# Kernel tuning notes

Hardware: AMD Instinct MI355X
Metric: run time of the kernel (lower is better)

The kernel has to match this reference:

```python
import jax, jax.numpy as jnp
import numpy as np

NUM_HEADS = 16
HEAD_DIM = 128
HIDDEN = 2048
C_KV = 512
C_Q = 1024
ROPE_DIM = 64
BATCH = 2
SEQ = 2048
ROPE_BASE = 10000.0


def _rope_cos_sin(seq_len, dim, dtype):
    # standard RoPE tables: [seq, dim] with concatenated (half, half) freqs
    inv_freq = 1.0 / (ROPE_BASE ** (jnp.arange(0, dim, 2, dtype=jnp.float32) / dim))
    t = jnp.arange(seq_len, dtype=jnp.float32)
    freqs = jnp.outer(t, inv_freq)                      # [S, dim/2]
    emb = jnp.concatenate([freqs, freqs], axis=-1)      # [S, dim]
    return jnp.cos(emb).astype(dtype), jnp.sin(emb).astype(dtype)


def _rotate_half(x):
    x1, x2 = jnp.split(x, 2, axis=-1)
    return jnp.concatenate([-x2, x1], axis=-1)


def _apply_rope(x, cos, sin):
    # x: [B, S, H, D]; cos/sin: [S, D] -> broadcast over batch and heads
    c = cos[None, :, None, :]
    s = sin[None, :, None, :]
    return x * c + _rotate_half(x) * s


def setup_inputs() -> dict:
    key = jax.random.key(0)
    ks = jax.random.split(key, 10)

    def xavier(k, shape):
        fan_in, fan_out = shape
        limit = np.sqrt(6.0 / (fan_in + fan_out))
        return jax.random.uniform(k, shape, jnp.float32, -limit, limit)

    hidden_states = jax.random.normal(ks[0], (BATCH, SEQ, HIDDEN), jnp.float32)
    # causal mask: 1 = masked out (positions j > i)
    causal = jnp.triu(jnp.ones((SEQ, SEQ), jnp.int32), k=1)
    mask = jnp.broadcast_to(causal[None, None], (BATCH, 1, SEQ, SEQ))
    return {
        "hidden_states": hidden_states,
        "mask": mask,
        "W_DKV": xavier(ks[1], (HIDDEN, C_KV)),
        "W_UK": xavier(ks[2], (C_KV, NUM_HEADS * HEAD_DIM)),
        "W_UV": xavier(ks[3], (C_KV, NUM_HEADS * HEAD_DIM)),
        "W_DQ": xavier(ks[4], (HIDDEN, C_Q)),
        "W_UQ": xavier(ks[5], (C_Q, NUM_HEADS * HEAD_DIM)),
        "W_QR": xavier(ks[6], (C_Q, NUM_HEADS * ROPE_DIM)),
        "W_KR": xavier(ks[7], (HIDDEN, ROPE_DIM)),
        "W_O": xavier(ks[8], (NUM_HEADS * HEAD_DIM, HIDDEN)),
    }


def reference(hidden_states, mask, W_DKV, W_UK, W_UV, W_DQ, W_UQ, W_QR, W_KR, W_O):
    B, S, _ = hidden_states.shape
    scale = 1.0 / jnp.sqrt(jnp.float32(HEAD_DIM + ROPE_DIM))

    c_KV = hidden_states @ W_DKV                         # [B,S,c_kv]
    k_C = (c_KV @ W_UK).reshape(B, S, NUM_HEADS, HEAD_DIM)
    v = (c_KV @ W_UV).reshape(B, S, NUM_HEADS, HEAD_DIM)
    c_Q = hidden_states @ W_DQ                           # [B,S,c_q]
    q_C = (c_Q @ W_UQ).reshape(B, S, NUM_HEADS, HEAD_DIM)
    q_R = (c_Q @ W_QR).reshape(B, S, NUM_HEADS, ROPE_DIM)
    k_R = (hidden_states @ W_KR).reshape(B, S, 1, ROPE_DIM)

    cos, sin = _rope_cos_sin(S, ROPE_DIM, hidden_states.dtype)
    q_R = _apply_rope(q_R, cos, sin)
    k_R = _apply_rope(k_R, cos, sin)
    k_R = jnp.broadcast_to(k_R, (B, S, NUM_HEADS, ROPE_DIM))

    q = jnp.concatenate([q_C, q_R], axis=-1)             # [B,S,H,D+R]
    k = jnp.concatenate([k_C, k_R], axis=-1)             # [B,S,H,D+R]

    scores = jnp.einsum('bqhd,bkhd->bhqk', q, k) * scale
    scores = scores + mask.astype(scores.dtype) * jnp.asarray(-1e9, scores.dtype)
    probs = jax.nn.softmax(scores, axis=-1)
    out = jnp.einsum('bhqk,bkhd->bqhd', probs, v).reshape(B, S, NUM_HEADS * HEAD_DIM)
    return out @ W_O
```

## Files before the change

kernel.cpp:

```cpp
#include <hip/hip_runtime.h>
#include <hip/hip_bf16.h>

typedef __bf16 bf16x8 __attribute__((ext_vector_type(8)));
typedef float f32x4 __attribute__((ext_vector_type(4)));
typedef float f32x16 __attribute__((ext_vector_type(16)));
using BF = __hip_bfloat16;

constexpr int B_   = 2;
constexpr int S_   = 2048;
constexpr int NH_  = 16;
constexpr int HD_  = 128;
constexpr int HID_ = 2048;
constexpr int CKV_ = 512;
constexpr int CQ_  = 1024;
constexpr int RD_  = 64;
constexpr int M_   = B_ * S_;
constexpr int DQK_ = HD_ + RD_;

__device__ __forceinline__ f32x4 mfma16(bf16x8 a, bf16x8 b, f32x4 c) {
  return __builtin_amdgcn_mfma_f32_16x16x32_bf16(a, b, c, 0, 0, 0);
}
__device__ __forceinline__ f32x16 mfma32(bf16x8 a, bf16x8 b, f32x16 c) {
  return __builtin_amdgcn_mfma_f32_32x32x16_bf16(a, b, c, 0, 0, 0);
}
__device__ __forceinline__ unsigned cvtpk(float a, float b) {
  unsigned r;
  asm("v_cvt_pk_bf16_f32 %0, %1, %2" : "=v"(r) : "v"(a), "v"(b));
  return r;
}
__device__ __forceinline__ void gload16(const void* g, void* lds) {
  __builtin_amdgcn_global_load_lds((const __attribute__((address_space(1))) void*)g,
                                   (__attribute__((address_space(3))) void*)lds,
                                   16, 0, 0);
}
__device__ __forceinline__ void plswap(unsigned& x, unsigned& y, bool hi) {
#if __has_builtin(__builtin_amdgcn_permlane32_swap)
  typedef unsigned u32x2 __attribute__((ext_vector_type(2)));
  u32x2 r = __builtin_amdgcn_permlane32_swap(x, y, false, false);
  x = r[0];
  y = r[1];
#else
  unsigned sx = (unsigned)__shfl_xor((int)x, 32, 64);
  unsigned sy = (unsigned)__shfl_xor((int)y, 32, 64);
  unsigned nx = hi ? sy : x;
  unsigned ny = hi ? y : sx;
  x = nx;
  y = ny;
#endif
}

__global__ __launch_bounds__(256) void f2b_kern(const float* __restrict__ in,
                                                BF* __restrict__ out, int n4) {
  int i = blockIdx.x * 256 + threadIdx.x;
  if (i >= n4) return;
  float4 v = reinterpret_cast<const float4*>(in)[i];
  BF o[4] = {__float2bfloat16(v.x), __float2bfloat16(v.y),
             __float2bfloat16(v.z), __float2bfloat16(v.w)};
  reinterpret_cast<uint2*>(out)[i] = *reinterpret_cast<uint2*>(o);
}

__global__ __launch_bounds__(256) void wtrans_all(const float* __restrict__ w0,
                                                  const float* __restrict__ w1,
                                                  const float* __restrict__ w2,
                                                  const float* __restrict__ w3,
                                                  const float* __restrict__ w4,
                                                  const float* __restrict__ w5,
                                                  const float* __restrict__ w6,
                                                  const float* __restrict__ w7,
                                                  BF* __restrict__ tCat1,
                                                  BF* __restrict__ tCat2,
                                                  BF* __restrict__ tCat3,
                                                  BF* __restrict__ tWO) {
  const int cum[9] = {0, 1024, 3072, 3328, 4352, 5376, 7424, 8448, 12544};
  const int nxt[8] = {16, 32, 4, 64, 64, 64, 32, 64};
  const int Kt[8]  = {2048, 2048, 2048, 512, 512, 1024, 1024, 2048};
  const int Nt[8]  = {512, 1024, 64, 2048, 2048, 2048, 1024, 2048};
  int bid = blockIdx.x;
  int j = 0;
#pragma unroll
  for (int t = 1; t < 8; t++)
    if (bid >= cum[t]) j = t;
  const float* in = (j == 0) ? w0 : (j == 1) ? w1 : (j == 2) ? w2 : (j == 3) ? w3
                   : (j == 4) ? w4 : (j == 5) ? w5 : (j == 6) ? w6 : w7;
  BF* out = (j == 0) ? tCat1 : (j == 1) ? tCat1 + (size_t)512 * 2048
           : (j == 2) ? tCat1 + (size_t)1536 * 2048
           : (j == 3) ? tCat2 : (j == 4) ? tCat2 + (size_t)2048 * 512
           : (j == 5) ? tCat3 : (j == 6) ? tCat3 + (size_t)2048 * 1024 : tWO;
  const int K = Kt[j], N = Nt[j];
  int rem = bid - cum[j];
  int bx = rem % nxt[j], by = rem / nxt[j];
  int n0 = bx * 32, k0 = by * 32;

  __shared__ float t[32][33];
  int tx = threadIdx.x, ty = threadIdx.y;
#pragma unroll
  for (int j4 = 0; j4 < 4; j4++) {
    int k = k0 + ty + j4 * 8, n = n0 + tx;
    t[ty + j4 * 8][tx] = (n < N) ? in[(size_t)k * N + n] : 0.f;
  }
  __syncthreads();
#pragma unroll
  for (int j4 = 0; j4 < 4; j4++) {
    int n = n0 + ty + j4 * 8, k = k0 + tx;
    out[(size_t)n * K + k] = __float2bfloat16(t[tx][ty + j4 * 8]);
  }
}

template <int F>
__global__ __launch_bounds__(256) void gemm_f(const BF* __restrict__ A,
                                              const BF* __restrict__ Bt,
                                              void* __restrict__ C0,
                                              void* __restrict__ C1,
                                              void* __restrict__ C2,
                                              int M, int N, int K) {
  __shared__ BF As[3][128][32];
  __shared__ BF Bs[3][128][32];
  const int tid = threadIdx.x;
  const int w = tid >> 6, l = tid & 63;
  const int lr = l & 15, lg = l >> 4;
  const int wr = w >> 1, wc = w & 1;
  const int gx = gridDim.x;
  const int nwg = gx * gridDim.y;
  const int f = blockIdx.y * gx + blockIdx.x;
  const int swz = (f & 7) * (nwg >> 3) + (f >> 3);
  const int m0 = (swz / gx) * 128, n0 = (swz % gx) * 128;

  f32x4 acc[4][4];
#pragma unroll
  for (int m = 0; m < 4; m++)
#pragma unroll
    for (int n = 0; n < 4; n++) acc[m][n] = (f32x4){0.f, 0.f, 0.f, 0.f};

  auto STAGE = [&](int buf, int k0) {
#pragma unroll
    for (int j = 0; j < 2; j++) {
      int idx = tid + j * 256;
      int row = idx >> 2, seg = idx & 3;
      gload16(A + (size_t)(m0 + row) * K + k0 + seg * 8, &As[buf][0][0] + idx * 8);
      gload16(Bt + (size_t)(n0 + row) * K + k0 + seg * 8, &Bs[buf][0][0] + idx * 8);
    }
  };

  const int nk = K >> 5;
  STAGE(0, 0);
  if (nk > 1) STAGE(1, 32);
  asm volatile("s_waitcnt vmcnt(4)" ::: "memory");
  __builtin_amdgcn_sched_barrier(0);
  __builtin_amdgcn_s_barrier();

  int cur = 0;
  for (int ki = 0; ki < nk; ki++) {
    bf16x8 af[4], bfr[4];
#pragma unroll
    for (int m = 0; m < 4; m++)
      af[m] = *reinterpret_cast<const bf16x8*>(&As[cur][wr * 64 + m * 16 + lr][lg * 8]);
#pragma unroll
    for (int n = 0; n < 4; n++)
      bfr[n] = *reinterpret_cast<const bf16x8*>(&Bs[cur][wc * 64 + n * 16 + lr][lg * 8]);
    if (ki + 2 < nk) {
      int nb = cur + 2; if (nb >= 3) nb -= 3;
      STAGE(nb, (ki + 2) << 5);
    }
    __builtin_amdgcn_sched_barrier(0);
    __builtin_amdgcn_s_setprio(1);
#pragma unroll
    for (int m = 0; m < 4; m++)
#pragma unroll
      for (int n = 0; n < 4; n++) acc[m][n] = mfma16(af[m], bfr[n], acc[m][n]);
    __builtin_amdgcn_s_setprio(0);
    __builtin_amdgcn_sched_barrier(0);
    if (ki + 1 < nk) {
      if (ki + 2 < nk) {
        asm volatile("s_waitcnt vmcnt(4)" ::: "memory");
      } else {
        asm volatile("s_waitcnt vmcnt(0)" ::: "memory");
      }
      __builtin_amdgcn_sched_barrier(0);
      __builtin_amdgcn_s_barrier();
    }
    cur = cur + 1; if (cur >= 3) cur = 0;
  }

#pragma unroll
  for (int m = 0; m < 4; m++) {
#pragma unroll
    for (int n = 0; n < 4; n++) {
#pragma unroll
      for (int j = 0; j < 4; j++) {
        int row = m0 + wr * 64 + m * 16 + lg * 4 + j;
        int col = n0 + wc * 64 + n * 16 + lr;
        float v = acc[m][n][j];
        if constexpr (F == 1) {
          if (col < 512)
            ((BF*)C0)[(size_t)row * 512 + col] = __float2bfloat16(v);
          else if (col < 1536)
            ((BF*)C1)[(size_t)row * 1024 + (col - 512)] = __float2bfloat16(v);
          else
            ((BF*)C2)[(size_t)row * 128 + (col - 1536)] = __float2bfloat16(v);
        } else {
          ((float*)C0)[(size_t)row * 2048 + col] = v;
        }
      }
    }
  }
}

__global__ __launch_bounds__(256) void gemm_f23(const BF* __restrict__ cQ,
                                                const BF* __restrict__ t3,
                                                BF* __restrict__ qbuf,
                                                BF* __restrict__ qRt,
                                                const BF* __restrict__ cKV,
                                                const BF* __restrict__ t2,
                                                BF* __restrict__ kbuf,
                                                BF* __restrict__ vTb) {
  __shared__ BF As[3][128][32];
  __shared__ BF Bs[3][128][32];
  const int tid = threadIdx.x;
  const int w = tid >> 6, l = tid & 63;
  const int lr = l & 15, lg = l >> 4;
  const int wr = w >> 1, wc = w & 1;
  const int f = blockIdx.y * 56 + blockIdx.x;
  const int swz = (f & 7) * (1792 >> 3) + (f >> 3);
  const int xt = swz % 56;
  const int m0 = (swz / 56) * 128;
  const bool isF3 = xt < 24;
  const BF* A  = isF3 ? cQ : cKV;
  const BF* Bt = isF3 ? t3 : t2;
  const int K  = isF3 ? 1024 : 512;
  const int n0 = (isF3 ? xt : xt - 24) * 128;

  f32x4 acc[4][4];
#pragma unroll
  for (int m = 0; m < 4; m++)
#pragma unroll
    for (int n = 0; n < 4; n++) acc[m][n] = (f32x4){0.f, 0.f, 0.f, 0.f};

  auto STAGE = [&](int buf, int k0) {
#pragma unroll
    for (int j = 0; j < 2; j++) {
      int idx = tid + j * 256;
      int row = idx >> 2, seg = idx & 3;
      gload16(A + (size_t)(m0 + row) * K + k0 + seg * 8, &As[buf][0][0] + idx * 8);
      gload16(Bt + (size_t)(n0 + row) * K + k0 + seg * 8, &Bs[buf][0][0] + idx * 8);
    }
  };

  const int nk = K >> 5;
  STAGE(0, 0);
  STAGE(1, 32);
  asm volatile("s_waitcnt vmcnt(4)" ::: "memory");
  __builtin_amdgcn_sched_barrier(0);
  __builtin_amdgcn_s_barrier();

  int cur = 0;
  for (int ki = 0; ki < nk; ki++) {
    bf16x8 af[4], bfr[4];
#pragma unroll
    for (int m = 0; m < 4; m++)
      af[m] = *reinterpret_cast<const bf16x8*>(&As[cur][wr * 64 + m * 16 + lr][lg * 8]);
#pragma unroll
    for (int n = 0; n < 4; n++)
      bfr[n] = *reinterpret_cast<const bf16x8*>(&Bs[cur][wc * 64 + n * 16 + lr][lg * 8]);
    if (ki + 2 < nk) {
      int nb = cur + 2; if (nb >= 3) nb -= 3;
      STAGE(nb, (ki + 2) << 5);
    }
    __builtin_amdgcn_sched_barrier(0);
    __builtin_amdgcn_s_setprio(1);
#pragma unroll
    for (int m = 0; m < 4; m++)
#pragma unroll
      for (int n = 0; n < 4; n++) acc[m][n] = mfma16(af[m], bfr[n], acc[m][n]);
    __builtin_amdgcn_s_setprio(0);
    __builtin_amdgcn_sched_barrier(0);
    if (ki + 1 < nk) {
      if (ki + 2 < nk) {
        asm volatile("s_waitcnt vmcnt(4)" ::: "memory");
      } else {
        asm volatile("s_waitcnt vmcnt(0)" ::: "memory");
      }
      __builtin_amdgcn_sched_barrier(0);
      __builtin_amdgcn_s_barrier();
    }
    cur = cur + 1; if (cur >= 3) cur = 0;
  }

#pragma unroll
  for (int m = 0; m < 4; m++) {
#pragma unroll
    for (int n = 0; n < 4; n++) {
#pragma unroll
      for (int j = 0; j < 4; j++) {
        int row = m0 + wr * 64 + m * 16 + lg * 4 + j;
        int col = n0 + wc * 64 + n * 16 + lr;
        float v = acc[m][n][j];
        int b = row >> 11, s = row & 2047;
        if (isF3) {
          if (col < 2048) {
            int h = col >> 7, d = col & 127;
            qbuf[((size_t)(b * 16 + h) * 2048 + s) * 192 + d] = __float2bfloat16(v);
          } else {
            qRt[(size_t)row * 1024 + (col - 2048)] = __float2bfloat16(v);
          }
        } else {
          if (col < 2048) {
            int h = col >> 7, d = col & 127;
            kbuf[((size_t)(b * 16 + h) * 2048 + s) * 192 + d] = __float2bfloat16(v);
          } else {
            int c2 = col - 2048, h = c2 >> 7, d = c2 & 127;
            vTb[((size_t)(b * 16 + h) * 128 + d) * 2048 + s] = __float2bfloat16(v);
          }
        }
      }
    }
  }
}

__global__ __launch_bounds__(256) void rope_q(const BF* __restrict__ qr, BF* __restrict__ qb) {
  int idx = blockIdx.x * 256 + threadIdx.x;
  int d = idx & 63, h = (idx >> 6) & 15, m = idx >> 10;
  int s = m & 2047, b = m >> 11;
  float x = __bfloat162float(qr[(size_t)(m << 10) + (h << 6) + d]);
  float other = __bfloat162float(qr[(size_t)(m << 10) + (h << 6) + (d ^ 32)]);
  float rot = (d < 32) ? -other : other;
  int di = d & 31;
  float arg = (float)s * powf(10000.f, -(float)di / 32.0f);
  float c = cosf(arg), sn = sinf(arg);
  qb[((size_t)(b * 16 + h) * 2048 + s) * 192 + 128 + d] = __float2bfloat16(x * c + rot * sn);
}

__global__ __launch_bounds__(256) void rope_k(const BF* __restrict__ kr, BF* __restrict__ kb) {
  int idx = blockIdx.x * 256 + threadIdx.x;
  int d = idx & 63, m = idx >> 6;
  int s = m & 2047, b = m >> 11;
  float x = __bfloat162float(kr[(size_t)m * 128 + d]);
  float other = __bfloat162float(kr[(size_t)m * 128 + (d ^ 32)]);
  float rot = (d < 32) ? -other : other;
  int di = d & 31;
  float arg = (float)s * powf(10000.f, -(float)di / 32.0f);
  float val = x * cosf(arg) + rot * sinf(arg);
  BF v = __float2bfloat16(val);
#pragma unroll
  for (int h = 0; h < 16; h++)
    kb[((size_t)(b * 16 + h) * 2048 + s) * 192 + 128 + d] = v;
}

__global__ __launch_bounds__(256, 2) void attn_kern(const BF* __restrict__ qb,
                                                    const BF* __restrict__ kb,
                                                    const BF* __restrict__ vT,
                                                    BF* __restrict__ o) {
  const int yy = blockIdx.y;
  const bool second = yy >= 16;
  const int bh = second ? ((yy - 16) * 2 + 1) : (yy * 2);
  const int qt = second ? (int)blockIdx.x : (15 - (int)blockIdx.x);
  const int q0 = qt * 128;
  const int tid = threadIdx.x;
  const int w = tid >> 6, l = tid & 63;
  const int lo5 = l & 31;
  const int hi = l >> 5;
  const int l7 = l & 7;

  __shared__ __align__(16) char smem[81920];

  const int q = q0 + w * 32 + lo5;
  const int qmax = q0 + w * 32 + 31;

  bf16x8 aq[12];
  {
    const BF* qrow = qb + ((size_t)bh * 2048 + q) * 192;
#pragma unroll
    for (int kst = 0; kst < 12; kst++)
      aq[kst] = *reinterpret_cast<const bf16x8*>(qrow + kst * 16 + hi * 8);
  }

  f32x16 Oacc[4];
#pragma unroll
  for (int dt = 0; dt < 4; dt++)
#pragma unroll
    for (int r = 0; r < 16; r++) Oacc[dt][r] = 0.f;
  float mrow = -3e38f, lrow = 0.f;

  const float scale = 0.07216878364870323f;
  const int nch = (q0 + 128) >> 6;

  auto STAGE = [&](int buf, int ch) {
    const int cc = ch << 6;
    BF* Ks = (BF*)(smem + buf * 40960);
    BF* Vs = (BF*)(smem + buf * 40960 + 24576);
#pragma unroll
    for (int j2 = 0; j2 < 6; j2++) {
      int D = tid + j2 * 256;
      int row = D / 24, sp = D % 24;
      int sl = sp ^ (row & 7);
      gload16(kb + ((size_t)bh * 2048 + cc + row) * 192 + sl * 8, Ks + D * 8);
    }
#pragma unroll
    for (int j2 = 0; j2 < 4; j2++) {
      int D = tid + j2 * 256;
      int row = D >> 3, sp = D & 7;
      int sl = sp ^ (row & 7);
      gload16(vT + ((size_t)bh * 128 + row) * 2048 + cc + sl * 8, Vs + D * 8);
    }
  };

  STAGE(0, 0);
  __syncthreads();

  for (int ch = 0; ch < nch; ch++) {
    const int c0 = ch << 6;
    const int cur = ch & 1;
    if (ch + 1 < nch) STAGE(cur ^ 1, ch + 1);
    __builtin_amdgcn_sched_barrier(0);
    BF* Ks = (BF*)(smem + cur * 40960);
    BF* Vs = (BF*)(smem + cur * 40960 + 24576);

    f32x16 sf[2];
    __builtin_amdgcn_s_setprio(1);
#pragma unroll
    for (int t = 0; t < 2; t++) {
      if (c0 + t * 32 <= qmax) {
        f32x16 a0, a1;
#pragma unroll
        for (int r = 0; r < 16; r++) { a0[r] = 0.f; a1[r] = 0.f; }
#pragma unroll
        for (int kst = 0; kst < 12; kst++) {
          bf16x8 kfr = *reinterpret_cast<const bf16x8*>(
              Ks + (t * 32 + lo5) * 192 + (((kst * 2 + hi) ^ l7) * 8));
          if (kst & 1) a1 = mfma32(kfr, aq[kst], a1);
          else         a0 = mfma32(kfr, aq[kst], a0);
        }
        sf[t] = a0 + a1;
      } else {
#pragma unroll
        for (int r = 0; r < 16; r++) sf[t][r] = 0.f;
      }
    }
    __builtin_amdgcn_s_setprio(0);

    float mx = -3e38f;
#pragma unroll
    for (int t = 0; t < 2; t++) {
#pragma unroll
      for (int r = 0; r < 16; r++) {
        int key = c0 + t * 32 + (r & 3) + 8 * (r >> 2) + 4 * hi;
        float v = sf[t][r] * scale;
        v = (key <= q) ? v : -1e30f;
        sf[t][r] = v;
        mx = fmaxf(mx, v);
      }
    }
    mx = fmaxf(mx, __shfl_xor(mx, 32, 64));
    float mnew = fmaxf(mrow, mx);
    float corr = __expf(mrow - mnew);
    mrow = mnew;
    float psum = 0.f;
#pragma unroll
    for (int t = 0; t < 2; t++)
#pragma unroll
      for (int r = 0; r < 16; r++) {
        float p = __expf(sf[t][r] - mnew);
        sf[t][r] = p;
        psum += p;
      }
    psum += __shfl_xor(psum, 32, 64);
    lrow = lrow * corr + psum;
#pragma unroll
    for (int dt = 0; dt < 4; dt++) Oacc[dt] *= corr;

    bf16x8 pb[4];
#pragma unroll
    for (int ks = 0; ks < 4; ks++) {
      if (c0 + ks * 16 > qmax) continue;
      int t = ks >> 1, base = (ks & 1) * 8;
      unsigned Xa = cvtpk(sf[t][base + 0], sf[t][base + 1]);
      unsigned Xb = cvtpk(sf[t][base + 2], sf[t][base + 3]);
      unsigned Ya = cvtpk(sf[t][base + 4], sf[t][base + 5]);
      unsigned Yb = cvtpk(sf[t][base + 6], sf[t][base + 7]);
      plswap(Xa, Ya, hi != 0);
      plswap(Xb, Yb, hi != 0);
      union { unsigned u[4]; bf16x8 v; } pk_;
      pk_.u[0] = Xa; pk_.u[1] = Xb; pk_.u[2] = Ya; pk_.u[3] = Yb;
      pb[ks] = pk_.v;
    }

    __builtin_amdgcn_s_setprio(1);
#pragma unroll
    for (int ks = 0; ks < 4; ks++) {
      if (c0 + ks * 16 > qmax) continue;
#pragma unroll
      for (int dt = 0; dt < 4; dt++) {
        bf16x8 vfr = *reinterpret_cast<const bf16x8*>(
            Vs + (dt * 32 + lo5) * 64 + (((ks * 2 + hi) ^ l7) * 8));
        Oacc[dt] = mfma32(vfr, pb[ks], Oacc[dt]);
      }
    }
    __builtin_amdgcn_s_setprio(0);
    __syncthreads();
  }

  BF* Osh = (BF*)smem;
  float rinv = 1.0f / lrow;
  const int orow = w * 32 + lo5;
#pragma unroll
  for (int dt = 0; dt < 4; dt++) {
#pragma unroll
    for (int g = 0; g < 4; g++) {
      unsigned d0 = cvtpk(Oacc[dt][g * 4 + 0] * rinv, Oacc[dt][g * 4 + 1] * rinv);
      unsigned d1 = cvtpk(Oacc[dt][g * 4 + 2] * rinv, Oacc[dt][g * 4 + 3] * rinv);
      uint2 pr; pr.x = d0; pr.y = d1;
      *reinterpret_cast<uint2*>(Osh + orow * 136 + dt * 32 + g * 8 + hi * 4) = pr;
    }
  }
  __syncthreads();
  const int b = bh >> 4, h = bh & 15;
  const int cb = tid & 15, rb = tid >> 4;
#pragma unroll
  for (int rr = 0; rr < 8; rr++) {
    int row = rb + rr * 16;
    bf16x8 v = *reinterpret_cast<const bf16x8*>(Osh + row * 136 + cb * 8);
    *reinterpret_cast<bf16x8*>(o + ((size_t)(b * 2048 + q0 + row)) * 2048 + h * 128 + cb * 8) = v;
  }
}

extern "C" void kernel_launch(void* const* d_in, const int* in_sizes, int n_in,
                              void* d_out, int out_size, void* d_ws, size_t ws_size,
                              hipStream_t stream) {
  const float* hs   = (const float*)d_in[0];
  const float* wDKV = (const float*)d_in[2];
  const float* wUK  = (const float*)d_in[3];
  const float* wUV  = (const float*)d_in[4];
  const float* wDQ  = (const float*)d_in[5];
  const float* wUQ  = (const float*)d_in[6];
  const float* wQR  = (const float*)d_in[7];
  const float* wKR  = (const float*)d_in[8];
  const float* wO   = (const float*)d_in[9];
  float* out = (float*)d_out;

  char* ws = (char*)d_ws;
  size_t off = 0;
  auto alloc = [&](size_t bytes) -> char* {
    char* p = ws + off;
    off += (bytes + 255) & ~(size_t)255;
    return p;
  };
  BF* hsb   = (BF*)alloc((size_t)M_ * HID_ * 2);
  BF* tCat1 = (BF*)alloc((size_t)1664 * HID_ * 2);
  BF* tCat2 = (BF*)alloc((size_t)4096 * CKV_ * 2);
  BF* tCat3 = (BF*)alloc((size_t)3072 * CQ_ * 2);
  BF* tWO   = (BF*)alloc((size_t)HID_ * (NH_*HD_) * 2);
  BF* cKV   = (BF*)alloc((size_t)M_ * CKV_ * 2);
  BF* cQ    = (BF*)alloc((size_t)M_ * CQ_ * 2);
  BF* qbuf  = (BF*)alloc((size_t)B_ * NH_ * S_ * DQK_ * 2);
  BF* kbuf  = (BF*)alloc((size_t)B_ * NH_ * S_ * DQK_ * 2);
  BF* vTb   = (BF*)alloc((size_t)B_ * NH_ * HD_ * S_ * 2);
  BF* qRt   = (BF*)alloc((size_t)M_ * (NH_*RD_) * 2);
  BF* kRt   = (BF*)alloc((size_t)M_ * 128 * 2);
  BF* aout  = (BF*)alloc((size_t)M_ * (NH_*HD_) * 2);

  f2b_kern<<<(M_ * HID_ / 4 + 255) / 256, 256, 0, stream>>>(hs, hsb, M_ * HID_ / 4);

  wtrans_all<<<12544, dim3(32, 8), 0, stream>>>(wDKV, wDQ, wKR, wUK, wUV, wUQ, wQR, wO,
                                                tCat1, tCat2, tCat3, tWO);

  gemm_f<1><<<dim3(1664 / 128, M_ / 128), 256, 0, stream>>>(hsb, tCat1, cKV, cQ, kRt, M_, 1664, HID_);
  gemm_f23<<<dim3(56, M_ / 128), 256, 0, stream>>>(cQ, tCat3, qbuf, qRt, cKV, tCat2, kbuf, vTb);

  rope_q<<<(M_ * NH_ * RD_) / 256, 256, 0, stream>>>(qRt, qbuf);
  rope_k<<<(M_ * RD_) / 256, 256, 0, stream>>>(kRt, kbuf);

  attn_kern<<<dim3(S_ / 128, B_ * NH_), 256, 0, stream>>>(qbuf, kbuf, vTb, aout);

  gemm_f<4><<<dim3(2048 / 128, M_ / 128), 256, 0, stream>>>(aout, tWO, out, nullptr, nullptr, M_, 2048, HID_);
}
```

Baseline: 316.2 us.

## Enlarge GEMM tiles to 256x128 and add lazy softmax rescaling in attention

All three GEMM kernels move from 128x128 to 256x128 output tiles. Each wave now computes 128x64 with 8x4 MFMA accumulators, which doubles A-tile staging and halves the grid. Separately, the flash-attention online softmax only rescales the running max, sum and output accumulator when some row's new max exceeds the old one by more than 8, which skips most rescale multiplies. The larger tiles raise register and LDS use, which may lower occupancy, and the grid shrinks to 208–896 blocks, which risks underfilling the GPU's CUs. The lazy rescale lets exponentials reach up to e^8, which could reduce precision in the bf16 P values.

```diff
diff --git a/kernel.cpp b/kernel.cpp
--- a/kernel.cpp
+++ b/kernel.cpp
@@ -113,47 +113,52 @@
                                               void* __restrict__ C1,
                                               void* __restrict__ C2,
                                               int M, int N, int K) {
-  __shared__ BF As[3][128][32];
+  __shared__ BF As[3][256][32];
   __shared__ BF Bs[3][128][32];
   const int tid = threadIdx.x;
   const int w = tid >> 6, l = tid & 63;
   const int lr = l & 15, lg = l >> 4;
   const int wr = w >> 1, wc = w & 1;
-  const int gx = gridDim.x;
-  const int nwg = gx * gridDim.y;
-  const int f = blockIdx.y * gx + blockIdx.x;
+  const int NT = gridDim.x;
+  const int nwg = NT * gridDim.y;
+  const int f = blockIdx.y * NT + blockIdx.x;
   const int swz = (f & 7) * (nwg >> 3) + (f >> 3);
-  const int m0 = (swz / gx) * 128, n0 = (swz % gx) * 128;
-
-  f32x4 acc[4][4];
-#pragma unroll
-  for (int m = 0; m < 4; m++)
+  const int m0 = (swz / NT) * 256, n0 = (swz % NT) * 128;
+
+  f32x4 acc[8][4];
+#pragma unroll
+  for (int m = 0; m < 8; m++)
 #pragma unroll
     for (int n = 0; n < 4; n++) acc[m][n] = (f32x4){0.f, 0.f, 0.f, 0.f};
 
   auto STAGE = [&](int buf, int k0) {
+#pragma unroll
+    for (int j = 0; j < 4; j++) {
+      int idx = tid + j * 256;
+      int row = idx >> 2, seg = idx & 3;
+      gload16(A + (size_t)(m0 + row) * K + k0 + seg * 8, &As[buf][0][0] + idx * 8);
+    }
 #pragma unroll
     for (int j = 0; j < 2; j++) {
       int idx = tid + j * 256;
       int row = idx >> 2, seg = idx & 3;
-      gload16(A + (size_t)(m0 + row) * K + k0 + seg * 8, &As[buf][0][0] + idx * 8);
       gload16(Bt + (size_t)(n0 + row) * K + k0 + seg * 8, &Bs[buf][0][0] + idx * 8);
     }
   };
 
   const int nk = K >> 5;
   STAGE(0, 0);
-  if (nk > 1) STAGE(1, 32);
-  asm volatile("s_waitcnt vmcnt(4)" ::: "memory");
+  STAGE(1, 32);
+  asm volatile("s_waitcnt vmcnt(6)" ::: "memory");
   __builtin_amdgcn_sched_barrier(0);
   __builtin_amdgcn_s_barrier();
 
   int cur = 0;
   for (int ki = 0; ki < nk; ki++) {
-    bf16x8 af[4], bfr[4];
-#pragma unroll
-    for (int m = 0; m < 4; m++)
-      af[m] = *reinterpret_cast<const bf16x8*>(&As[cur][wr * 64 + m * 16 + lr][lg * 8]);
+    bf16x8 af[8], bfr[4];
+#pragma unroll
+    for (int m = 0; m < 8; m++)
+      af[m] = *reinterpret_cast<const bf16x8*>(&As[cur][wr * 128 + m * 16 + lr][lg * 8]);
 #pragma unroll
     for (int n = 0; n < 4; n++)
       bfr[n] = *reinterpret_cast<const bf16x8*>(&Bs[cur][wc * 64 + n * 16 + lr][lg * 8]);
@@ -164,14 +169,14 @@
     __builtin_amdgcn_sched_barrier(0);
     __builtin_amdgcn_s_setprio(1);
 #pragma unroll
-    for (int m = 0; m < 4; m++)
+    for (int m = 0; m < 8; m++)
 #pragma unroll
       for (int n = 0; n < 4; n++) acc[m][n] = mfma16(af[m], bfr[n], acc[m][n]);
     __builtin_amdgcn_s_setprio(0);
     __builtin_amdgcn_sched_barrier(0);
     if (ki + 1 < nk) {
       if (ki + 2 < nk) {
-        asm volatile("s_waitcnt vmcnt(4)" ::: "memory");
+        asm volatile("s_waitcnt vmcnt(6)" ::: "memory");
       } else {
         asm volatile("s_waitcnt vmcnt(0)" ::: "memory");
       }
@@ -182,12 +187,12 @@
   }
 
 #pragma unroll
-  for (int m = 0; m < 4; m++) {
+  for (int m = 0; m < 8; m++) {
 #pragma unroll
     for (int n = 0; n < 4; n++) {
 #pragma unroll
       for (int j = 0; j < 4; j++) {
-        int row = m0 + wr * 64 + m * 16 + lg * 4 + j;
+        int row = m0 + wr * 128 + m * 16 + lg * 4 + j;
         int col = n0 + wc * 64 + n * 16 + lr;
         float v = acc[m][n][j];
         if constexpr (F == 1) {
@@ -213,34 +218,39 @@
                                                 const BF* __restrict__ t2,
                                                 BF* __restrict__ kbuf,
                                                 BF* __restrict__ vTb) {
-  __shared__ BF As[3][128][32];
+  __shared__ BF As[3][256][32];
   __shared__ BF Bs[3][128][32];
   const int tid = threadIdx.x;
   const int w = tid >> 6, l = tid & 63;
   const int lr = l & 15, lg = l >> 4;
   const int wr = w >> 1, wc = w & 1;
   const int f = blockIdx.y * 56 + blockIdx.x;
-  const int swz = (f & 7) * (1792 >> 3) + (f >> 3);
+  const int swz = (f & 7) * (896 >> 3) + (f >> 3);
   const int xt = swz % 56;
-  const int m0 = (swz / 56) * 128;
+  const int m0 = (swz / 56) * 256;
   const bool isF3 = xt < 24;
   const BF* A  = isF3 ? cQ : cKV;
   const BF* Bt = isF3 ? t3 : t2;
   const int K  = isF3 ? 1024 : 512;
   const int n0 = (isF3 ? xt : xt - 24) * 128;
 
-  f32x4 acc[4][4];
-#pragma unroll
-  for (int m = 0; m < 4; m++)
+  f32x4 acc[8][4];
+#pragma unroll
+  for (int m = 0; m < 8; m++)
 #pragma unroll
     for (int n = 0; n < 4; n++) acc[m][n] = (f32x4){0.f, 0.f, 0.f, 0.f};
 
   auto STAGE = [&](int buf, int k0) {
+#pragma unroll
+    for (int j = 0; j < 4; j++) {
+      int idx = tid + j * 256;
+      int row = idx >> 2, seg = idx & 3;
+      gload16(A + (size_t)(m0 + row) * K + k0 + seg * 8, &As[buf][0][0] + idx * 8);
+    }
 #pragma unroll
     for (int j = 0; j < 2; j++) {
       int idx = tid + j * 256;
       int row = idx >> 2, seg = idx & 3;
-      gload16(A + (size_t)(m0 + row) * K + k0 + seg * 8, &As[buf][0][0] + idx * 8);
       gload16(Bt + (size_t)(n0 + row) * K + k0 + seg * 8, &Bs[buf][0][0] + idx * 8);
     }
   };
@@ -248,16 +258,16 @@
   const int nk = K >> 5;
   STAGE(0, 0);
   STAGE(1, 32);
-  asm volatile("s_waitcnt vmcnt(4)" ::: "memory");
+  asm volatile("s_waitcnt vmcnt(6)" ::: "memory");
   __builtin_amdgcn_sched_barrier(0);
   __builtin_amdgcn_s_barrier();
 
   int cur = 0;
   for (int ki = 0; ki < nk; ki++) {
-    bf16x8 af[4], bfr[4];
-#pragma unroll
-    for (int m = 0; m < 4; m++)
-      af[m] = *reinterpret_cast<const bf16x8*>(&As[cur][wr * 64 + m * 16 + lr][lg * 8]);
+    bf16x8 af[8], bfr[4];
+#pragma unroll
+    for (int m = 0; m < 8; m++)
+      af[m] = *reinterpret_cast<const bf16x8*>(&As[cur][wr * 128 + m * 16 + lr][lg * 8]);
 #pragma unroll
     for (int n = 0; n < 4; n++)
       bfr[n] = *reinterpret_cast<const bf16x8*>(&Bs[cur][wc * 64 + n * 16 + lr][lg * 8]);
@@ -268,14 +278,14 @@
     __builtin_amdgcn_sched_barrier(0);
     __builtin_amdgcn_s_setprio(1);
 #pragma unroll
-    for (int m = 0; m < 4; m++)
+    for (int m = 0; m < 8; m++)
 #pragma unroll
       for (int n = 0; n < 4; n++) acc[m][n] = mfma16(af[m], bfr[n], acc[m][n]);
     __builtin_amdgcn_s_setprio(0);
     __builtin_amdgcn_sched_barrier(0);
     if (ki + 1 < nk) {
       if (ki + 2 < nk) {
-        asm volatile("s_waitcnt vmcnt(4)" ::: "memory");
+        asm volatile("s_waitcnt vmcnt(6)" ::: "memory");
       } else {
         asm volatile("s_waitcnt vmcnt(0)" ::: "memory");
       }
@@ -286,12 +296,12 @@
   }
 
 #pragma unroll
-  for (int m = 0; m < 4; m++) {
+  for (int m = 0; m < 8; m++) {
 #pragma unroll
     for (int n = 0; n < 4; n++) {
 #pragma unroll
       for (int j = 0; j < 4; j++) {
-        int row = m0 + wr * 64 + m * 16 + lg * 4 + j;
+        int row = m0 + wr * 128 + m * 16 + lg * 4 + j;
         int col = n0 + wc * 64 + n * 16 + lr;
         float v = acc[m][n][j];
         int b = row >> 11, s = row & 2047;
@@ -450,22 +460,25 @@
       }
     }
     mx = fmaxf(mx, __shfl_xor(mx, 32, 64));
-    float mnew = fmaxf(mrow, mx);
-    float corr = __expf(mrow - mnew);
-    mrow = mnew;
+    if (!__all(mx - mrow <= 8.0f)) {
+      float mnew = fmaxf(mrow, mx);
+      float corr = __expf(mrow - mnew);
+      mrow = mnew;
+      lrow *= corr;
+#pragma unroll
+      for (int dt = 0; dt < 4; dt++) Oacc[dt] *= corr;
+    }
     float psum = 0.f;
 #pragma unroll
     for (int t = 0; t < 2; t++)
 #pragma unroll
       for (int r = 0; r < 16; r++) {
-        float p = __expf(sf[t][r] - mnew);
+        float p = __expf(sf[t][r] - mrow);
         sf[t][r] = p;
         psum += p;
       }
     psum += __shfl_xor(psum, 32, 64);
-    lrow = lrow * corr + psum;
-#pragma unroll
-    for (int dt = 0; dt < 4; dt++) Oacc[dt] *= corr;
+    lrow += psum;
 
     bf16x8 pb[4];
 #pragma unroll
@@ -562,13 +575,13 @@
   wtrans_all<<<12544, dim3(32, 8), 0, stream>>>(wDKV, wDQ, wKR, wUK, wUV, wUQ, wQR, wO,
                                                 tCat1, tCat2, tCat3, tWO);
 
-  gemm_f<1><<<dim3(1664 / 128, M_ / 128), 256, 0, stream>>>(hsb, tCat1, cKV, cQ, kRt, M_, 1664, HID_);
-  gemm_f23<<<dim3(56, M_ / 128), 256, 0, stream>>>(cQ, tCat3, qbuf, qRt, cKV, tCat2, kbuf, vTb);
+  gemm_f<1><<<dim3(13, 16), 256, 0, stream>>>(hsb, tCat1, cKV, cQ, kRt, M_, 1664, HID_);
+  gemm_f23<<<dim3(56, 16), 256, 0, stream>>>(cQ, tCat3, qbuf, qRt, cKV, tCat2, kbuf, vTb);
 
   rope_q<<<(M_ * NH_ * RD_) / 256, 256, 0, stream>>>(qRt, qbuf);
   rope_k<<<(M_ * RD_) / 256, 256, 0, stream>>>(kRt, kbuf);
 
   attn_kern<<<dim3(S_ / 128, B_ * NH_), 256, 0, stream>>>(qbuf, kbuf, vTb, aout);
 
-  gemm_f<4><<<dim3(2048 / 128, M_ / 128), 256, 0, stream>>>(aout, tWO, out, nullptr, nullptr, M_, 2048, HID_);
-}
+  gemm_f<4><<<dim3(16, 16), 256, 0, stream>>>(aout, tWO, out, nullptr, nullptr, M_, 2048, HID_);
+}
```

Result: slower. 377.4 us (+19.3%).
